# Performance work log

Hardware: AMD Instinct MI355X
Metric: run time of the kernel (lower is better)

The kernel has to match this reference:

```python
import jax, jax.numpy as jnp
import numpy as np

B, K, FM, TS, H, W = 128, 24, 24, 11, 40, 40
EPS = 1e-6


def setup_inputs() -> dict:
    key = jax.random.key(0)
    ks = jax.random.split(key, 8)

    def w(k, shape):
        fan_in = float(np.prod(shape[2:]))
        return jax.random.normal(k, shape, jnp.float32) / np.float32(np.sqrt(fan_in))

    return {
        "x": jax.random.normal(ks[0], (B, 1, H, W), jnp.float32),
        "noise": jax.random.uniform(ks[1], (B, K), jnp.float32, -2.0, 2.0),
        "W1": w(ks[2], (K, 128, 1, 3, 3)), "b1": jnp.zeros((K, 128), jnp.float32),
        "W2": w(ks[3], (K, 128, 128, 3, 3)), "b2": jnp.zeros((K, 128), jnp.float32),
        "W3": w(ks[4], (K, 128, 128, 3, 3)), "b3": jnp.zeros((K, 128), jnp.float32),
        "W4": w(ks[5], (K, 128, 128, 3, 3)), "b4": jnp.zeros((K, 128), jnp.float32),
        "W5": w(ks[6], (K, FM, 128, 1, 1)), "b5": jnp.zeros((K, FM), jnp.float32),
        "templates": jax.random.normal(ks[7], (K, TS, TS), jnp.float32),
    }


def _conv(x, w, b, s):
    y = jax.lax.conv_general_dilated(x, w, (s, s), 'VALID',
                                     dimension_numbers=('NCHW', 'OIHW', 'NCHW'))
    return y + b[None, :, None, None]


def _inv_affine_mats(pose):
    # pose [B,K,6]: angle(deg), tx, ty, scale, shear_x(deg), shear_y(deg)
    # torchvision-style inverse affine matrix (maps output canvas coords -> template coords)
    ang = jnp.deg2rad(pose[..., 0])
    tx, ty = pose[..., 1], pose[..., 2]
    sc = pose[..., 3] + EPS
    sx = jnp.deg2rad(pose[..., 4])
    sy = jnp.deg2rad(pose[..., 5])
    a = jnp.cos(ang - sy) / jnp.cos(sy)
    b = -jnp.cos(ang - sy) * jnp.tan(sx) / jnp.cos(sy) - jnp.sin(ang)
    c = jnp.sin(ang - sy) / jnp.cos(sy)
    d = -jnp.sin(ang - sy) * jnp.tan(sx) / jnp.cos(sy) + jnp.cos(ang)
    m00, m01, m10, m11 = d / sc, -b / sc, -c / sc, a / sc
    cx = cy = (TS - 1) * 0.5
    m02 = m00 * (-cx - tx) + m01 * (-cy - ty) + cx
    m12 = m10 * (-cx - tx) + m11 * (-cy - ty) + cy
    return m00, m01, m02, m10, m11, m12


def _warp_templates(templates, pose):
    # Fused affine warp + resize-to-(H,W), bilinear, zero fill (batched grid_sample).
    m00, m01, m02, m10, m11, m12 = _inv_affine_mats(pose)  # each [B,K]
    ys, xs = jnp.meshgrid(jnp.arange(H, dtype=jnp.float32),
                          jnp.arange(W, dtype=jnp.float32), indexing='ij')
    u = (xs + 0.5) * (TS / W) - 0.5  # output pixel -> template-canvas x
    v = (ys + 0.5) * (TS / H) - 0.5
    src_x = m00[..., None, None] * u + m01[..., None, None] * v + m02[..., None, None]
    src_y = m10[..., None, None] * u + m11[..., None, None] * v + m12[..., None, None]

    def sample(tmpl, sx_, sy_):  # tmpl [TS,TS]; sx_,sy_ [B,H,W]
        x0 = jnp.floor(sx_); y0 = jnp.floor(sy_)
        wx = sx_ - x0; wy = sy_ - y0
        x0i = x0.astype(jnp.int32); y0i = y0.astype(jnp.int32)

        def tap(yi, xi):
            ok = (xi >= 0) & (xi < TS) & (yi >= 0) & (yi < TS)
            val = tmpl[jnp.clip(yi, 0, TS - 1), jnp.clip(xi, 0, TS - 1)]
            return jnp.where(ok, val, 0.0)

        v00 = tap(y0i, x0i); v01 = tap(y0i, x0i + 1)
        v10 = tap(y0i + 1, x0i); v11 = tap(y0i + 1, x0i + 1)
        return (v00 * (1 - wx) + v01 * wx) * (1 - wy) + (v10 * (1 - wx) + v11 * wx) * wy

    return jax.vmap(sample, in_axes=(0, 1, 1), out_axes=1)(templates, src_x, src_y)  # [B,K,H,W]


def _forward(x, noise, W1, b1, W2, b2, W3, b3, W4, b4, W5, b5, templates):
    def capsule(w1, bb1, w2, bb2, w3, bb3, w4, bb4, w5, bb5):
        h = jax.nn.relu(_conv(x, w1, bb1, 2))
        h = jax.nn.relu(_conv(h, w2, bb2, 2))
        h = jax.nn.relu(_conv(h, w3, bb3, 1))
        h = jax.nn.relu(_conv(h, w4, bb4, 1))
        return _conv(h, w5, bb5, 1)

    outs = jax.vmap(capsule)(W1, b1, W2, b2, W3, b3, W4, b4, W5, b5)  # [K,B,FM,h,w]
    att = outs[:, :, -1]  # [K,B,h,w]
    hs, ws = att.shape[-2:]
    att = jax.nn.softmax(att.reshape(K, B, hs * ws), axis=-1).reshape(K, B, hs, ws)
    pooled = jnp.einsum('kbfhw,kbhw->bkf', outs[:, :, :-1], att)  # [B,K,FM-1]

    x_m = jax.nn.relu(pooled[:, :, :6])                        # [B,K,6] pose
    d_m = jax.nn.sigmoid(pooled[:, :, 6] + noise)[..., None]   # [B,K,1] presence
    c_z = jax.nn.relu(pooled[:, :, 7:])                        # [B,K,16]

    tt = _warp_templates(templates, x_m)                       # [B,K,H,W]
    mix_prob = jax.nn.softmax(d_m * tt.reshape(B, K, H * W), axis=2).reshape(B, K, H, W)

    std = jnp.std(x.reshape(B, 1, -1), axis=-1, ddof=1)[:, None]   # [B,1,1] (unbiased, as torch)
    mult = (1.0 / jnp.sqrt(std * 2.0 * jnp.pi))[..., None]         # [B,1,1,1] (as written in source)
    pmul = (-1.0 / (2.0 * std ** 2))[..., None]                    # [B,1,1,1]
    xd = jax.lax.stop_gradient(x)                                  # detach_x = x.data
    gaussians = mult * jnp.exp((xd - tt) ** 2 * pmul)              # [B,K,H,W]
    ll = jnp.log(jnp.sum(gaussians * mix_prob, axis=1)).sum((-1, -2)).mean()

    x_m_det = jax.lax.stop_gradient(x_m)
    d_m_det = jax.lax.stop_gradient(d_m)
    tmpl_det = jnp.broadcast_to(jax.lax.stop_gradient(templates).reshape(1, K, TS * TS),
                                (B, K, TS * TS))
    input_ocae = jnp.concatenate([d_m_det, x_m_det, tmpl_det, c_z], axis=-1)  # [B,K,144]
    return ll, input_ocae, x_m_det, d_m_det


def reference(x, noise, W1, b1, W2, b2, W3, b3, W4, b4, W5, b5, templates):
    return _forward(x, noise, W1, b1, W2, b2, W3, b3, W4, b4, W5, b5, templates)
```

## Files before the change

kernel.cpp:

```cpp
#include <hip/hip_runtime.h>
#include <math.h>

typedef __attribute__((ext_vector_type(8))) short bf16x8;
typedef __attribute__((ext_vector_type(4))) float f32x4;
typedef __attribute__((ext_vector_type(16))) float f32x16;
typedef unsigned int uint32;
typedef unsigned short ushort;

namespace {
constexpr int KK = 24, BB = 128;

constexpr size_t SZ_W1P = (size_t)24 * 128 * 32 * 2;
constexpr size_t SZ_W5P = (size_t)24 * 32 * 128 * 2;
constexpr size_t SZ_WB  = (size_t)24 * 128 * 1152 * 2;
constexpr size_t OFF_W1P = 0;
constexpr size_t OFF_W5P = OFF_W1P + SZ_W1P;
constexpr size_t OFF_WB2 = OFF_W5P + SZ_W5P;
constexpr size_t OFF_WB3 = OFF_WB2 + SZ_WB;
constexpr size_t OFF_WB4 = OFF_WB3 + SZ_WB;
constexpr size_t OFF_TT  = OFF_WB4 + SZ_WB;
constexpr size_t SZ_TT   = (size_t)128 * 24 * 1600 * 2;
constexpr size_t OFF_SMAX = OFF_TT + SZ_TT;
constexpr size_t OFF_SDEN = OFF_SMAX + 12288;
constexpr size_t OFF_DM   = OFF_SDEN + 12288;
constexpr size_t OFF_PART = OFF_DM + 12288;

constexpr long long O_OCAE = 1;
constexpr long long O_XM   = O_OCAE + (long long)BB * KK * 144;
constexpr long long O_DM   = O_XM + (long long)BB * KK * 6;

constexpr int R1_SZ   = 80864;
constexpr int XIM_OFF = 0;
constexpr int H1T_OFF = 23104;
constexpr int XSB_OFF = 74464;
constexpr int H2S_OFF = 0;
constexpr int H3S_OFF = 0;
constexpr int H4B_OFF = 31392;
constexpr int OUTS_OFF = 0;
constexpr int ATT_OFF = 4800;
constexpr int PS_OFF  = 5000;
}

__device__ inline ushort f2bf(float f) {
  uint32 u = __builtin_bit_cast(uint32, f);
  u += 0x7fffu + ((u >> 16) & 1u);
  return (ushort)(u >> 16);
}
__device__ inline float bf2f(ushort u) {
  return __builtin_bit_cast(float, (uint32)u << 16);
}
__device__ inline uint32 cvtpk(float a, float b) {
  uint32 r;
  asm("v_cvt_pk_bf16_f32 %0, %1, %2" : "=v"(r) : "v"(a), "v"(b));
  return r;
}
__device__ inline void bar_lds() {
  asm volatile("s_waitcnt lgkmcnt(0)\n\ts_barrier" ::: "memory");
}

__global__ __launch_bounds__(128) void k_w1p(const float* __restrict__ W1,
                                             const float* __restrict__ W5,
                                             const float* __restrict__ b1,
                                             ushort* __restrict__ W1p,
                                             ushort* __restrict__ W5p) {
  const int k = blockIdx.x, t = threadIdx.x;
  {
    ushort tmp[32];
    #pragma unroll
    for (int i = 0; i < 32; ++i) tmp[i] = 0;
    #pragma unroll
    for (int j = 0; j < 9; ++j) tmp[j] = f2bf(W1[(k * 128 + t) * 9 + j]);
    tmp[9] = f2bf(b1[k * 128 + t]);
    uint4* dp = (uint4*)(W1p + ((size_t)k * 128 + t) * 32);
    #pragma unroll
    for (int i = 0; i < 4; ++i) dp[i] = ((uint4*)tmp)[i];
  }
  if (t < 32) {
    ushort* dp = W5p + ((size_t)k * 32 + t) * 128;
    if (t < 24) {
      const float* sp = W5 + (size_t)k * 3072 + t * 128;
      for (int ci = 0; ci < 128; ++ci) dp[ci] = f2bf(sp[ci]);
    } else {
      for (int ci = 0; ci < 128; ++ci) dp[ci] = 0;
    }
  }
}

__global__ __launch_bounds__(256) void k_wp(
    const float* __restrict__ W2, const float* __restrict__ W3, const float* __restrict__ W4,
    ushort* __restrict__ W2p, ushort* __restrict__ W3p, ushort* __restrict__ W4p) {
  const int blk = blockIdx.x;
  const int sel = blk / 384;
  const int bb = blk - sel * 384;
  const float* src = (sel == 0) ? W2 : (sel == 1) ? W3 : W4;
  ushort* dst = (sel == 0) ? W2p : (sel == 1) ? W3p : W4p;
  const int k = bb >> 4;
  const int co = ((bb & 15) << 3) + (threadIdx.x >> 5);
  const int cil = threadIdx.x & 31;
  #pragma unroll
  for (int c = 0; c < 4; ++c) {
    const float* sp = src + ((size_t)(k * 128 + co) * 128 + c * 32 + cil) * 9;
    float v[9];
    #pragma unroll
    for (int j = 0; j < 9; ++j) v[j] = sp[j];
    ushort* dp = dst + (size_t)(k * 4 + c) * 9 * 128 * 32;
    #pragma unroll
    for (int j = 0; j < 9; ++j) dp[(j * 128 + co) * 32 + cil] = f2bf(v[j]);
  }
}

__device__ inline float tapf(const float* tm, int yi, int xi) {
  const bool ok = (xi >= 0) & (xi < 11) & (yi >= 0) & (yi < 11);
  const int yc = min(max(yi, 0), 10), xc = min(max(xi, 0), 10);
  const float v = tm[yc * 11 + xc];
  return ok ? v : 0.0f;
}

__global__ __launch_bounds__(256, 2) void k_tower(
    const float* __restrict__ x, const ushort* __restrict__ W1p,
    const ushort* __restrict__ W2p, const float* __restrict__ b2,
    const ushort* __restrict__ W3p, const float* __restrict__ b3,
    const ushort* __restrict__ W4p, const float* __restrict__ b4,
    const ushort* __restrict__ W5p, const float* __restrict__ b5,
    const float* __restrict__ noise, const float* __restrict__ templates,
    float* __restrict__ out, ushort* __restrict__ ttb,
    float* __restrict__ smax, float* __restrict__ sden, float* __restrict__ dmw)
{
  const int bi = blockIdx.x;
  const int blk = (bi & 7) * 192 + (bi >> 3);
  const int kb0 = blk * 2;
  const int k = kb0 >> 7;
  const int b0 = kb0 & 127;
  const int t = threadIdx.x;

  __shared__ __align__(16) char R1[R1_SZ];
  __shared__ float red[8];
  __shared__ float b5s[24];
  __shared__ float tm[121];

  ushort* xim = (ushort*)(R1 + XIM_OFF);
  ushort* h1T = (ushort*)(R1 + H1T_OFF);
  ushort* xsb = (ushort*)(R1 + XSB_OFF);
  char* h2sb = R1 + H2S_OFF;
  char* h3sb = R1 + H3S_OFF;
  ushort* h4b = (ushort*)(R1 + H4B_OFF);
  float*  outs_s = (float*)(R1 + OUTS_OFF);
  float*  att_s  = (float*)(R1 + ATT_OFF);
  float*  ps  = (float*)(R1 + PS_OFF);

  for (int i = t; i < 800; i += 256) {
    const int im = i / 400, j = i - im * 400;
    const float4 v = ((const float4*)(x + (size_t)(b0 + im) * 1600))[j];
    uint2 pk;
    pk.x = cvtpk(v.x, v.y);
    pk.y = cvtpk(v.z, v.w);
    *(uint2*)(xsb + im * 1600 + 4 * j) = pk;
  }
  bar_lds();

  for (int f = t; f < 722; f += 256) {
    const int im = f / 361, fl = f - im * 361;
    const int py = fl / 19, px = fl - 19 * py;
    const ushort* bp = xsb + im * 1600 + py * 80 + px * 2;
    const uint32 t0 = bp[0], t1 = bp[1], t2 = bp[2];
    const uint32 t3 = bp[40], t4 = bp[41], t5 = bp[42];
    const uint32 t6 = bp[80], t7 = bp[81], t8 = bp[82];
    uint4* dp = (uint4*)(xim + (im * 361 + fl) * 16);
    dp[0] = make_uint4(t0 | (t1 << 16), t2 | (t3 << 16), t4 | (t5 << 16), t6 | (t7 << 16));
    dp[1] = make_uint4(t8 | 0x3F800000u, 0u, 0u, 0u);
  }

  const int w = t >> 6, lane = t & 63, r = lane & 15, s = lane >> 4;
  const int l31 = lane & 31, kh = lane >> 5;
  const int img = w >> 1;
  const int wi  = w & 1;
  const int m0  = wi * 64;

  ushort* xim_i = xim + img * 5776;
  ushort* h1T_i = h1T + img * 14440;
  char* h1Tb_i = (char*)h1T_i;
  char* h2s_i = h2sb + img * 25920;
  char* h3s_i = h3sb + img * 15680;
  ushort* h4b_i = h4b + img * 3400;

  {
    int bb2[3];
    #pragma unroll
    for (int nt = 0; nt < 3; ++nt) {
      const int n = 32 * nt + l31;
      const int py = n / 9, px = n - 9 * py;
      bb2[nt] = ((n < 81) ? (38 * py + 2 * px) * 80 : 0) + 16 * kh;
    }

    f32x16 acc[2][3];
    #pragma unroll
    for (int mt = 0; mt < 2; ++mt)
      #pragma unroll
      for (int nt = 0; nt < 3; ++nt) acc[mt][nt] = (f32x16)(0.f);

    const ushort* W2k = W2p + (size_t)k * 147456 + (m0 + l31) * 32 + 8 * kh;
    const ushort* W1k = W1p + ((size_t)k * 128 + l31) * 32 + 8 * kh;

    for (int c = 0; c < 4; ++c) {
      bar_lds();
      {
        const bf16x8 a1 = *(const bf16x8*)(W1k + c * 1024);
        #pragma unroll
        for (int nt2 = 0; nt2 < 6; ++nt2) {
          const int n = (wi * 6 + nt2) * 32 + l31;
          const int pos = (n < 361) ? n : 360;
          const bf16x8 bv = *(const bf16x8*)(xim_i + pos * 16 + 8 * kh);
          f32x16 cc = __builtin_amdgcn_mfma_f32_32x32x16_bf16(a1, bv, (f32x16)(0.f), 0, 0, 0);
          if (n < 361) {
            #pragma unroll
            for (int q = 0; q < 4; ++q) {
              const int cil = 8 * q + 4 * kh;
              uint2 pk;
              pk.x = cvtpk(fmaxf(cc[4 * q + 0], 0.f), fmaxf(cc[4 * q + 1], 0.f));
              pk.y = cvtpk(fmaxf(cc[4 * q + 2], 0.f), fmaxf(cc[4 * q + 3], 0.f));
              *(uint2*)(h1T_i + n * 40 + cil) = pk;
            }
          }
        }
      }
      bar_lds();
      const ushort* Abase = W2k + (size_t)c * 36864;
      bf16x8 Ag[2][12];
      #pragma unroll
      for (int q = 0; q < 12; ++q)
        Ag[0][q] = *(const bf16x8*)(Abase + (size_t)(q >> 2) * 4096 + (q & 1) * 1024 + ((q >> 1) & 1) * 16);
      #pragma unroll
      for (int g = 0; g < 3; ++g) {
        if (g < 2) {
          #pragma unroll
          for (int q = 0; q < 12; ++q)
            Ag[(g + 1) & 1][q] = *(const bf16x8*)(Abase + (size_t)(3 * (g + 1) + (q >> 2)) * 4096 + (q & 1) * 1024 + ((q >> 1) & 1) * 16);
        }
        #pragma unroll
        for (int jj = 0; jj < 3; ++jj) {
          const int j = 3 * g + jj;
          const int off80 = ((j / 3) * 19 + (j - 3 * (j / 3))) * 80;
          bf16x8 Bv[2][3];
          #pragma unroll
          for (int h = 0; h < 2; ++h)
            #pragma unroll
            for (int nt = 0; nt < 3; ++nt)
              Bv[h][nt] = *(const bf16x8*)(h1Tb_i + bb2[nt] + off80 + 32 * h);
          #pragma unroll
          for (int h = 0; h < 2; ++h)
            #pragma unroll
            for (int mt = 0; mt < 2; ++mt)
              #pragma unroll
              for (int nt = 0; nt < 3; ++nt)
                acc[mt][nt] = __builtin_amdgcn_mfma_f32_32x32x16_bf16(
                    Ag[g & 1][jj * 4 + h * 2 + mt], Bv[h][nt], acc[mt][nt], 0, 0, 0);
        }
      }
    }
    bar_lds();
    #pragma unroll
    for (int mt = 0; mt < 2; ++mt)
      #pragma unroll
      for (int nt = 0; nt < 3; ++nt) {
        const int p = 32 * nt + l31;
        if (p < 81) {
          #pragma unroll
          for (int q = 0; q < 4; ++q) {
            const int co0 = m0 + 32 * mt + 8 * q + 4 * kh;
            const float4 bv = *(const float4*)(b2 + k * 128 + co0);
            const int c2 = co0 >> 5, cil = co0 & 31;
            uint2 pk;
            pk.x = cvtpk(fmaxf(acc[mt][nt][4 * q + 0] + bv.x, 0.f), fmaxf(acc[mt][nt][4 * q + 1] + bv.y, 0.f));
            pk.y = cvtpk(fmaxf(acc[mt][nt][4 * q + 2] + bv.z, 0.f), fmaxf(acc[mt][nt][4 * q + 3] + bv.w, 0.f));
            *(uint2*)(h2s_i + ((c2 * 81 + p) * 40 + cil) * 2) = pk;
          }
        }
      }
  }
  bar_lds();

  {
    int bb3[2];
    #pragma unroll
    for (int nt = 0; nt < 2; ++nt) {
      const int n = 32 * nt + l31;
      const int py = n / 7, px = n - 7 * py;
      bb3[nt] = ((n < 49) ? (9 * py + px) * 80 : 0) + 16 * kh;
    }
    f32x16 acc[2][2];
    #pragma unroll
    for (int mt = 0; mt < 2; ++mt)
      #pragma unroll
      for (int nt = 0; nt < 2; ++nt) acc[mt][nt] = (f32x16)(0.f);

    const ushort* W3k = W3p + (size_t)k * 147456 + (m0 + l31) * 32 + 8 * kh;
    for (int c = 0; c < 4; ++c) {
      const ushort* Abase = W3k + (size_t)c * 36864;
      const char* h2c = h2s_i + c * 6480;
      bf16x8 Ag[2][12];
      #pragma unroll
      for (int q = 0; q < 12; ++q)
        Ag[0][q] = *(const bf16x8*)(Abase + (size_t)(q >> 2) * 4096 + (q & 1) * 1024 + ((q >> 1) & 1) * 16);
      #pragma unroll
      for (int g = 0; g < 3; ++g) {
        if (g < 2) {
          #pragma unroll
          for (int q = 0; q < 12; ++q)
            Ag[(g + 1) & 1][q] = *(const bf16x8*)(Abase + (size_t)(3 * (g + 1) + (q >> 2)) * 4096 + (q & 1) * 1024 + ((q >> 1) & 1) * 16);
        }
        #pragma unroll
        for (int jj = 0; jj < 3; ++jj) {
          const int j = 3 * g + jj;
          const int off80 = ((j / 3) * 9 + (j - 3 * (j / 3))) * 80;
          bf16x8 Bv[2][2];
          #pragma unroll
          for (int h = 0; h < 2; ++h)
            #pragma unroll
            for (int nt = 0; nt < 2; ++nt)
              Bv[h][nt] = *(const bf16x8*)(h2c + bb3[nt] + off80 + 32 * h);
          #pragma unroll
          for (int h = 0; h < 2; ++h)
            #pragma unroll
            for (int mt = 0; mt < 2; ++mt)
              #pragma unroll
              for (int nt = 0; nt < 2; ++nt)
                acc[mt][nt] = __builtin_amdgcn_mfma_f32_32x32x16_bf16(
                    Ag[g & 1][jj * 4 + h * 2 + mt], Bv[h][nt], acc[mt][nt], 0, 0, 0);
        }
      }
    }
    bar_lds();
    #pragma unroll
    for (int mt = 0; mt < 2; ++mt)
      #pragma unroll
      for (int nt = 0; nt < 2; ++nt) {
        const int p = 32 * nt + l31;
        if (p < 49) {
          #pragma unroll
          for (int q = 0; q < 4; ++q) {
            const int co0 = m0 + 32 * mt + 8 * q + 4 * kh;
            const float4 bv = *(const float4*)(b3 + k * 128 + co0);
            const int c2 = co0 >> 5, cil = co0 & 31;
            uint2 pk;
            pk.x = cvtpk(fmaxf(acc[mt][nt][4 * q + 0] + bv.x, 0.f), fmaxf(acc[mt][nt][4 * q + 1] + bv.y, 0.f));
            pk.y = cvtpk(fmaxf(acc[mt][nt][4 * q + 2] + bv.z, 0.f), fmaxf(acc[mt][nt][4 * q + 3] + bv.w, 0.f));
            *(uint2*)(h3s_i + ((c2 * 49 + p) * 40 + cil) * 2) = pk;
          }
        }
      }
    for (int i = t; i < 121; i += 256) tm[i] = templates[k * 121 + i];
  }
  bar_lds();

  {
    const int n4 = l31;
    const int py4 = n4 / 5, px4 = n4 - 5 * py4;
    const int bb4 = ((n4 < 25) ? (7 * py4 + px4) * 80 : 0) + 16 * kh;
    f32x16 acc[2];
    acc[0] = (f32x16)(0.f);
    acc[1] = (f32x16)(0.f);

    const ushort* W4k = W4p + (size_t)k * 147456 + (m0 + l31) * 32 + 8 * kh;
    for (int c = 0; c < 4; ++c) {
      const ushort* Abase = W4k + (size_t)c * 36864;
      const char* h3c = h3s_i + c * 3920;
      bf16x8 Ag[2][12];
      #pragma unroll
      for (int q = 0; q < 12; ++q)
        Ag[0][q] = *(const bf16x8*)(Abase + (size_t)(q >> 2) * 4096 + (q & 1) * 1024 + ((q >> 1) & 1) * 16);
      #pragma unroll
      for (int g = 0; g < 3; ++g) {
        if (g < 2) {
          #pragma unroll
          for (int q = 0; q < 12; ++q)
            Ag[(g + 1) & 1][q] = *(const bf16x8*)(Abase + (size_t)(3 * (g + 1) + (q >> 2)) * 4096 + (q & 1) * 1024 + ((q >> 1) & 1) * 16);
        }
        #pragma unroll
        for (int jj = 0; jj < 3; ++jj) {
          const int j = 3 * g + jj;
          const int off80 = ((j / 3) * 7 + (j - 3 * (j / 3))) * 80;
          bf16x8 Bv[2];
          #pragma unroll
          for (int h = 0; h < 2; ++h)
            Bv[h] = *(const bf16x8*)(h3c + bb4 + off80 + 32 * h);
          #pragma unroll
          for (int h = 0; h < 2; ++h)
            #pragma unroll
            for (int mt = 0; mt < 2; ++mt)
              acc[mt] = __builtin_amdgcn_mfma_f32_32x32x16_bf16(
                  Ag[g & 1][jj * 4 + h * 2 + mt], Bv[h], acc[mt], 0, 0, 0);
        }
      }
    }
    bar_lds();
    #pragma unroll
    for (int mt = 0; mt < 2; ++mt) {
      const int p = l31;
      if (p < 25) {
        #pragma unroll
        for (int q = 0; q < 4; ++q) {
          const int co0 = m0 + 32 * mt + 8 * q + 4 * kh;
          const float4 bv = *(const float4*)(b4 + k * 128 + co0);
          uint2 pk;
          pk.x = cvtpk(fmaxf(acc[mt][4 * q + 0] + bv.x, 0.f), fmaxf(acc[mt][4 * q + 1] + bv.y, 0.f));
          pk.y = cvtpk(fmaxf(acc[mt][4 * q + 2] + bv.z, 0.f), fmaxf(acc[mt][4 * q + 3] + bv.w, 0.f));
          *(uint2*)(h4b_i + p * 136 + co0) = pk;
        }
      }
    }
    if (t < 24) b5s[t] = b5[k * 24 + t];
  }
  bar_lds();

  {
    const int mt = wi;
    f32x4 acc5[2];
    acc5[0] = (f32x4){0.f, 0.f, 0.f, 0.f};
    acc5[1] = (f32x4){0.f, 0.f, 0.f, 0.f};
    const ushort* A5 = W5p + ((size_t)k * 32 + mt * 16 + r) * 128 + 8 * s;
    #pragma unroll
    for (int ks = 0; ks < 4; ++ks) {
      const bf16x8 a5 = *(const bf16x8*)(A5 + ks * 32);
      #pragma unroll
      for (int nt = 0; nt < 2; ++nt) {
        const int p = 16 * nt + r;
        const int pv = (p < 25) ? p : 0;
        const bf16x8 bv = *(const bf16x8*)(h4b_i + pv * 136 + ks * 32 + 8 * s);
        acc5[nt] = __builtin_amdgcn_mfma_f32_16x16x32_bf16(a5, bv, acc5[nt], 0, 0, 0);
      }
    }
    #pragma unroll
    for (int nt = 0; nt < 2; ++nt) {
      const int p = 16 * nt + r;
      if (p < 25) {
        #pragma unroll
        for (int rg = 0; rg < 4; ++rg) {
          const int fm = mt * 16 + 4 * s + rg;
          if (fm < 24) outs_s[img * 600 + fm * 25 + p] = acc5[nt][rg] + b5s[fm];
        }
      }
    }
  }
  bar_lds();

  if (!(t & 64)) {
    const int im = t >> 7;
    const int tl = t & 63;
    float v = (tl < 25) ? outs_s[im * 600 + 575 + tl] : -1e30f;
    #pragma unroll
    for (int off = 32; off; off >>= 1) v = fmaxf(v, __shfl_xor(v, off));
    const float m = v;
    float e = (tl < 25) ? expf(outs_s[im * 600 + 575 + tl] - m) : 0.0f;
    float ss = e;
    #pragma unroll
    for (int off = 32; off; off >>= 1) ss += __shfl_xor(ss, off);
    if (tl < 25) att_s[im * 25 + tl] = e / ss;
  }
  bar_lds();

  {
    const int im = t >> 7;
    const int tl = t & 127;
    if (tl < 23) {
      float v = 0.f;
      #pragma unroll
      for (int p = 0; p < 25; ++p) v = fmaf(outs_s[im * 600 + tl * 25 + p], att_s[im * 25 + p], v);
      ps[im * 23 + tl] = v;
    }
  }
  bar_lds();

  float dmv[2];
  #pragma unroll
  for (int im = 0; im < 2; ++im) {
    const int idx = (b0 + im) * KK + k;
    const float dl = ps[im * 23 + 6] + noise[idx];
    dmv[im] = 1.0f / (1.0f + expf(-dl));
  }

  #pragma unroll
  for (int im = 0; im < 2; ++im) {
    const int idx = (b0 + im) * KK + k;
    if (t < 144) {
      float v;
      if (t == 0)       v = dmv[im];
      else if (t < 7)   v = fmaxf(ps[im * 23 + t - 1], 0.0f);
      else if (t < 128) v = tm[t - 7];
      else              v = fmaxf(ps[im * 23 + 7 + (t - 128)], 0.0f);
      out[O_OCAE + (size_t)idx * 144 + t] = v;
    }
    if (t < 6) out[O_XM + (size_t)idx * 6 + t] = fmaxf(ps[im * 23 + t], 0.0f);
    if (t == 0) out[O_DM + idx] = dmv[im];
  }

  const int im = t >> 7;
  const int tl = t & 127;
  const int idx = (b0 + im) * KK + k;
  const float dm = dmv[im];

  const float D2R = 0.017453292519943295f;
  const float ang = fmaxf(ps[im * 23 + 0], 0.0f) * D2R;
  const float tx = fmaxf(ps[im * 23 + 1], 0.0f), ty = fmaxf(ps[im * 23 + 2], 0.0f);
  const float sc = fmaxf(ps[im * 23 + 3], 0.0f) + 1e-6f;
  const float sxr = fmaxf(ps[im * 23 + 4], 0.0f) * D2R;
  const float syr = fmaxf(ps[im * 23 + 5], 0.0f) * D2R;
  const float cas = cosf(ang - syr), sas = sinf(ang - syr);
  const float csy = cosf(syr), tsx = tanf(sxr);
  const float a_ = cas / csy;
  const float b_ = -cas * tsx / csy - sinf(ang);
  const float c_ = sas / csy;
  const float d_ = -sas * tsx / csy + cosf(ang);
  const float m00 = d_ / sc, m01 = -b_ / sc, m10 = -c_ / sc, m11 = a_ / sc;
  const float m02 = m00 * (-5.0f - tx) + m01 * (-5.0f - ty) + 5.0f;
  const float m12 = m10 * (-5.0f - tx) + m11 * (-5.0f - ty) + 5.0f;

  const float S = 0.275f;
  float ttv[13];
  float lmax = -1e30f;
  #pragma unroll
  for (int i = 0; i < 13; ++i) {
    const int pix = tl + 128 * i;
    float val2 = 0.0f;
    if (pix < 1600) {
      const int py = pix / 40, px = pix - 40 * py;
      const float u = (px + 0.5f) * S - 0.5f;
      const float v = (py + 0.5f) * S - 0.5f;
      const float sx = m00 * u + m01 * v + m02;
      const float sy = m10 * u + m11 * v + m12;
      const float x0 = floorf(sx), y0 = floorf(sy);
      const float wx = sx - x0, wy = sy - y0;
      const int xi = (int)x0, yi = (int)y0;
      const float v00 = tapf(tm, yi, xi);
      const float v01 = tapf(tm, yi, xi + 1);
      const float v10 = tapf(tm, yi + 1, xi);
      const float v11 = tapf(tm, yi + 1, xi + 1);
      const float val = (v00 * (1.0f - wx) + v01 * wx) * (1.0f - wy) + (v10 * (1.0f - wx) + v11 * wx) * wy;
      const ushort tb = f2bf(val);
      val2 = bf2f(tb);
      ttb[(size_t)idx * 1600 + pix] = tb;
      lmax = fmaxf(lmax, dm * val2);
    }
    ttv[i] = val2;
  }

  #pragma unroll
  for (int off = 32; off; off >>= 1) lmax = fmaxf(lmax, __shfl_xor(lmax, off));
  if ((t & 63) == 0) red[t >> 6] = lmax;
  bar_lds();
  const float m = fmaxf(red[2 * im], red[2 * im + 1]);
  float ls = 0.0f;
  #pragma unroll
  for (int i = 0; i < 13; ++i)
    if (tl + 128 * i < 1600) ls += expf(fmaf(dm, ttv[i], -m));
  #pragma unroll
  for (int off = 32; off; off >>= 1) ls += __shfl_xor(ls, off);
  bar_lds();
  if ((t & 63) == 0) red[4 + (t >> 6)] = ls;
  bar_lds();
  if ((t & 127) == 0) {
    smax[idx] = m;
    sden[idx] = red[4 + 2 * im] + red[5 + 2 * im];
    dmw[idx] = dm;
  }
}

__global__ __launch_bounds__(256) void k_ll(
    const float* __restrict__ x, const ushort* __restrict__ ttb,
    const float* __restrict__ smax, const float* __restrict__ sden,
    const float* __restrict__ dmw, float* __restrict__ part)
{
  const int b = blockIdx.x >> 2;
  const int chunk = blockIdx.x & 3;
  const int t = threadIdx.x;

  __shared__ __align__(16) float xs[1600];
  __shared__ float kd[24], km[24], ki[24];
  __shared__ float red[4], red2[4];

  for (int i = t; i < 400; i += 256)
    ((float4*)xs)[i] = ((const float4*)(x + (size_t)b * 1600))[i];
  if (t < 24) {
    kd[t] = dmw[b * 24 + t];
    km[t] = smax[b * 24 + t];
    ki[t] = 1.0f / sden[b * 24 + t];
  }
  __syncthreads();

  float s1 = 0.f, s2 = 0.f;
  for (int i = t; i < 1600; i += 256) { const float v = xs[i]; s1 += v; s2 = fmaf(v, v, s2); }
  #pragma unroll
  for (int off = 32; off; off >>= 1) { s1 += __shfl_xor(s1, off); s2 += __shfl_xor(s2, off); }
  if ((t & 63) == 0) { red[t >> 6] = s1; red2[t >> 6] = s2; }
  __syncthreads();
  s1 = red[0] + red[1] + red[2] + red[3];
  s2 = red2[0] + red2[1] + red2[2] + red2[3];
  const float var = (s2 - s1 * s1 * (1.0f / 1600.0f)) * (1.0f / 1599.0f);
  const float stdv = sqrtf(var);
  const float mult = 1.0f / sqrtf(stdv * 6.283185307179586f);
  const float pmul = -1.0f / (2.0f * stdv * stdv);

  const int p0 = chunk * 400;
  float ll = 0.0f;
  for (int ii = t; ii < 400; ii += 256) {
    const int pix = p0 + ii;
    const float xv = xs[pix];
    float sum = 0.0f;
    #pragma unroll 6
    for (int kk2 = 0; kk2 < 24; ++kk2) {
      const float tv = bf2f(ttb[(size_t)(b * 24 + kk2) * 1600 + pix]);
      const float dxv = xv - tv;
      sum += expf(fmaf(dxv * dxv, pmul, fmaf(kd[kk2], tv, -km[kk2]))) * ki[kk2];
    }
    ll += logf(mult * sum);
  }
  #pragma unroll
  for (int off = 32; off; off >>= 1) ll += __shfl_xor(ll, off);
  __syncthreads();
  if ((t & 63) == 0) red[t >> 6] = ll;
  __syncthreads();
  if (t == 0) part[blockIdx.x] = red[0] + red[1] + red[2] + red[3];
}

__global__ void k_final(const float* __restrict__ part, float* __restrict__ out)
{
  const int t = threadIdx.x;
  float v = part[t] + part[t + 256];
  #pragma unroll
  for (int off = 32; off; off >>= 1) v += __shfl_xor(v, off);
  __shared__ float red[4];
  if ((t & 63) == 0) red[t >> 6] = v;
  __syncthreads();
  if (t == 0) out[0] = (red[0] + red[1] + red[2] + red[3]) * (1.0f / 128.0f);
}

extern "C" void kernel_launch(void* const* d_in, const int* in_sizes, int n_in,
                              void* d_out, int out_size, void* d_ws, size_t ws_size,
                              hipStream_t stream)
{
  const float* x     = (const float*)d_in[0];
  const float* noise = (const float*)d_in[1];
  const float* W1    = (const float*)d_in[2];
  const float* b1    = (const float*)d_in[3];
  const float* W2    = (const float*)d_in[4];
  const float* b2    = (const float*)d_in[5];
  const float* W3    = (const float*)d_in[6];
  const float* b3    = (const float*)d_in[7];
  const float* W4    = (const float*)d_in[8];
  const float* b4    = (const float*)d_in[9];
  const float* W5    = (const float*)d_in[10];
  const float* b5    = (const float*)d_in[11];
  const float* tmpl  = (const float*)d_in[12];
  float* out = (float*)d_out;
  char* wsb = (char*)d_ws;

  ushort* W1p = (ushort*)(wsb + OFF_W1P);
  ushort* W5p = (ushort*)(wsb + OFF_W5P);
  ushort* W2p = (ushort*)(wsb + OFF_WB2);
  ushort* W3p = (ushort*)(wsb + OFF_WB3);
  ushort* W4p = (ushort*)(wsb + OFF_WB4);
  ushort* ttp  = (ushort*)(wsb + OFF_TT);
  float* smaxp = (float*)(wsb + OFF_SMAX);
  float* sdenp = (float*)(wsb + OFF_SDEN);
  float* dmp   = (float*)(wsb + OFF_DM);
  float* partp = (float*)(wsb + OFF_PART);

  k_w1p<<<24, 128, 0, stream>>>(W1, W5, b1, W1p, W5p);
  k_wp<<<1152, 256, 0, stream>>>(W2, W3, W4, W2p, W3p, W4p);
  k_tower<<<KK * BB / 2, 256, 0, stream>>>(x, W1p, W2p, b2, W3p, b3, W4p, b4,
                                           W5p, b5, noise, tmpl, out, ttp, smaxp, sdenp, dmp);
  k_ll<<<BB * 4, 256, 0, stream>>>(x, ttp, smaxp, sdenp, dmp, partp);
  k_final<<<1, 256, 0, stream>>>(partp, out);
}
```

Baseline: 233.1 us.

## Switch conv2-4 tower to FP8 weights/activations with scaled 32x32x64 MFMA

Converts the W2-W4 weights to FP8 (e4m3) in the pre-pack kernel and stores the h1/h2/h3 intermediate activations in LDS as FP8. The conv layers now use mfma_scale 32x32x64 f8f6f4 instructions with unit scales, covering 64 input channels per instruction instead of 16. The goal is to halve weight and LDS traffic and cut the MFMA instruction count. The cost is lower numerical precision, which risks tolerance failures. The LDS layouts and the conv1 work split across waves are also reorganised.

```diff
diff --git a/kernel.cpp b/kernel.cpp
--- a/kernel.cpp
+++ b/kernel.cpp
@@ -4,15 +4,18 @@
 typedef __attribute__((ext_vector_type(8))) short bf16x8;
 typedef __attribute__((ext_vector_type(4))) float f32x4;
 typedef __attribute__((ext_vector_type(16))) float f32x16;
+typedef __attribute__((ext_vector_type(4))) int i32x4;
+typedef __attribute__((ext_vector_type(8))) int i32x8;
 typedef unsigned int uint32;
 typedef unsigned short ushort;
+typedef unsigned char uchar;
 
 namespace {
 constexpr int KK = 24, BB = 128;
 
 constexpr size_t SZ_W1P = (size_t)24 * 128 * 32 * 2;
 constexpr size_t SZ_W5P = (size_t)24 * 32 * 128 * 2;
-constexpr size_t SZ_WB  = (size_t)24 * 128 * 1152 * 2;
+constexpr size_t SZ_WB  = (size_t)24 * 2 * 9 * 128 * 64;
 constexpr size_t OFF_W1P = 0;
 constexpr size_t OFF_W5P = OFF_W1P + SZ_W1P;
 constexpr size_t OFF_WB2 = OFF_W5P + SZ_W5P;
@@ -57,6 +60,16 @@
 __device__ inline void bar_lds() {
   asm volatile("s_waitcnt lgkmcnt(0)\n\ts_barrier" ::: "memory");
 }
+__device__ inline uint32 pk4fp8(float a, float b, float c, float d) {
+  int u = __builtin_amdgcn_cvt_pk_fp8_f32(fmaxf(a, 0.f), fmaxf(b, 0.f), 0, false);
+  u = __builtin_amdgcn_cvt_pk_fp8_f32(fmaxf(c, 0.f), fmaxf(d, 0.f), u, true);
+  return (uint32)u;
+}
+__device__ inline i32x8 ldB8(const char* p) {
+  i32x4 lo = *(const i32x4*)(p);
+  i32x4 hi = *(const i32x4*)(p + 16);
+  return __builtin_shufflevector(lo, hi, 0, 1, 2, 3, 4, 5, 6, 7);
+}
 
 __global__ __launch_bounds__(128) void k_w1p(const float* __restrict__ W1,
                                              const float* __restrict__ W5,
@@ -88,12 +101,12 @@
 
 __global__ __launch_bounds__(256) void k_wp(
     const float* __restrict__ W2, const float* __restrict__ W3, const float* __restrict__ W4,
-    ushort* __restrict__ W2p, ushort* __restrict__ W3p, ushort* __restrict__ W4p) {
+    uchar* __restrict__ W2p, uchar* __restrict__ W3p, uchar* __restrict__ W4p) {
   const int blk = blockIdx.x;
   const int sel = blk / 384;
   const int bb = blk - sel * 384;
   const float* src = (sel == 0) ? W2 : (sel == 1) ? W3 : W4;
-  ushort* dst = (sel == 0) ? W2p : (sel == 1) ? W3p : W4p;
+  uchar* dst = (sel == 0) ? W2p : (sel == 1) ? W3p : W4p;
   const int k = bb >> 4;
   const int co = ((bb & 15) << 3) + (threadIdx.x >> 5);
   const int cil = threadIdx.x & 31;
@@ -103,9 +116,10 @@
     float v[9];
     #pragma unroll
     for (int j = 0; j < 9; ++j) v[j] = sp[j];
-    ushort* dp = dst + (size_t)(k * 4 + c) * 9 * 128 * 32;
-    #pragma unroll
-    for (int j = 0; j < 9; ++j) dp[(j * 128 + co) * 32 + cil] = f2bf(v[j]);
+    uchar* dp = dst + (size_t)(k * 2 + (c >> 1)) * 9 * 8192 + co * 64 + (c & 1) * 32 + cil;
+    #pragma unroll
+    for (int j = 0; j < 9; ++j)
+      dp[(size_t)j * 8192] = (uchar)(__builtin_amdgcn_cvt_pk_fp8_f32(v[j], v[j], 0, false) & 0xFF);
   }
 }
 
@@ -118,9 +132,9 @@
 
 __global__ __launch_bounds__(256, 2) void k_tower(
     const float* __restrict__ x, const ushort* __restrict__ W1p,
-    const ushort* __restrict__ W2p, const float* __restrict__ b2,
-    const ushort* __restrict__ W3p, const float* __restrict__ b3,
-    const ushort* __restrict__ W4p, const float* __restrict__ b4,
+    const uchar* __restrict__ W2p, const float* __restrict__ b2,
+    const uchar* __restrict__ W3p, const float* __restrict__ b3,
+    const uchar* __restrict__ W4p, const float* __restrict__ b4,
     const ushort* __restrict__ W5p, const float* __restrict__ b5,
     const float* __restrict__ noise, const float* __restrict__ templates,
     float* __restrict__ out, ushort* __restrict__ ttb,
@@ -139,8 +153,8 @@
   __shared__ float tm[121];
 
   ushort* xim = (ushort*)(R1 + XIM_OFF);
-  ushort* h1T = (ushort*)(R1 + H1T_OFF);
   ushort* xsb = (ushort*)(R1 + XSB_OFF);
+  char* h1Tall = R1 + H1T_OFF;
   char* h2sb = R1 + H2S_OFF;
   char* h3sb = R1 + H3S_OFF;
   ushort* h4b = (ushort*)(R1 + H4B_OFF);
@@ -170,17 +184,17 @@
     dp[1] = make_uint4(t8 | 0x3F800000u, 0u, 0u, 0u);
   }
 
-  const int w = t >> 6, lane = t & 63, r = lane & 15, s = lane >> 4;
+  const int w = t >> 6, lane = t & 63;
+  const int r = lane & 15, s = lane >> 4;
   const int l31 = lane & 31, kh = lane >> 5;
   const int img = w >> 1;
   const int wi  = w & 1;
   const int m0  = wi * 64;
 
   ushort* xim_i = xim + img * 5776;
-  ushort* h1T_i = h1T + img * 14440;
-  char* h1Tb_i = (char*)h1T_i;
-  char* h2s_i = h2sb + img * 25920;
-  char* h3s_i = h3sb + img * 15680;
+  char* h1Tb_i = h1Tall + img * 28880;
+  char* h2s_i = h2sb + img * 12960;
+  char* h3s_i = h3sb + img * 7840;
   ushort* h4b_i = h4b + img * 3400;
 
   {
@@ -189,7 +203,7 @@
     for (int nt = 0; nt < 3; ++nt) {
       const int n = 32 * nt + l31;
       const int py = n / 9, px = n - 9 * py;
-      bb2[nt] = ((n < 81) ? (38 * py + 2 * px) * 80 : 0) + 16 * kh;
+      bb2[nt] = ((n < 81) ? (38 * py + 2 * px) * 80 : 0) + 32 * kh;
     }
 
     f32x16 acc[2][3];
@@ -198,63 +212,51 @@
       #pragma unroll
       for (int nt = 0; nt < 3; ++nt) acc[mt][nt] = (f32x16)(0.f);
 
-    const ushort* W2k = W2p + (size_t)k * 147456 + (m0 + l31) * 32 + 8 * kh;
+    const uchar* W2k = W2p + ((size_t)k * 2) * 9 * 8192 + (m0 + l31) * 64 + 32 * kh;
     const ushort* W1k = W1p + ((size_t)k * 128 + l31) * 32 + 8 * kh;
 
-    for (int c = 0; c < 4; ++c) {
+    for (int cp = 0; cp < 2; ++cp) {
       bar_lds();
       {
-        const bf16x8 a1 = *(const bf16x8*)(W1k + c * 1024);
-        #pragma unroll
-        for (int nt2 = 0; nt2 < 6; ++nt2) {
-          const int n = (wi * 6 + nt2) * 32 + l31;
+        const bf16x8 a1 = *(const bf16x8*)(W1k + (2 * cp + wi) * 1024);
+        #pragma unroll
+        for (int nt2 = 0; nt2 < 12; ++nt2) {
+          const int n = nt2 * 32 + l31;
           const int pos = (n < 361) ? n : 360;
           const bf16x8 bv = *(const bf16x8*)(xim_i + pos * 16 + 8 * kh);
           f32x16 cc = __builtin_amdgcn_mfma_f32_32x32x16_bf16(a1, bv, (f32x16)(0.f), 0, 0, 0);
           if (n < 361) {
             #pragma unroll
             for (int q = 0; q < 4; ++q) {
-              const int cil = 8 * q + 4 * kh;
-              uint2 pk;
-              pk.x = cvtpk(fmaxf(cc[4 * q + 0], 0.f), fmaxf(cc[4 * q + 1], 0.f));
-              pk.y = cvtpk(fmaxf(cc[4 * q + 2], 0.f), fmaxf(cc[4 * q + 3], 0.f));
-              *(uint2*)(h1T_i + n * 40 + cil) = pk;
+              const uint32 u = pk4fp8(cc[4 * q], cc[4 * q + 1], cc[4 * q + 2], cc[4 * q + 3]);
+              *(uint32*)(h1Tb_i + n * 80 + 32 * wi + 8 * q + 4 * kh) = u;
             }
           }
         }
       }
       bar_lds();
-      const ushort* Abase = W2k + (size_t)c * 36864;
-      bf16x8 Ag[2][12];
-      #pragma unroll
-      for (int q = 0; q < 12; ++q)
-        Ag[0][q] = *(const bf16x8*)(Abase + (size_t)(q >> 2) * 4096 + (q & 1) * 1024 + ((q >> 1) & 1) * 16);
-      #pragma unroll
-      for (int g = 0; g < 3; ++g) {
-        if (g < 2) {
+      const uchar* Abase = W2k + (size_t)cp * 9 * 8192;
+      i32x8 Af[2][2];
+      #pragma unroll
+      for (int mt = 0; mt < 2; ++mt) Af[0][mt] = *(const i32x8*)(Abase + mt * 2048);
+      #pragma unroll
+      for (int j = 0; j < 9; ++j) {
+        if (j < 8) {
           #pragma unroll
-          for (int q = 0; q < 12; ++q)
-            Ag[(g + 1) & 1][q] = *(const bf16x8*)(Abase + (size_t)(3 * (g + 1) + (q >> 2)) * 4096 + (q & 1) * 1024 + ((q >> 1) & 1) * 16);
-        }
-        #pragma unroll
-        for (int jj = 0; jj < 3; ++jj) {
-          const int j = 3 * g + jj;
-          const int off80 = ((j / 3) * 19 + (j - 3 * (j / 3))) * 80;
-          bf16x8 Bv[2][3];
+          for (int mt = 0; mt < 2; ++mt)
+            Af[(j + 1) & 1][mt] = *(const i32x8*)(Abase + (size_t)(j + 1) * 8192 + mt * 2048);
+        }
+        const int off80 = ((j / 3) * 19 + (j - 3 * (j / 3))) * 80;
+        i32x8 Bv[3];
+        #pragma unroll
+        for (int nt = 0; nt < 3; ++nt)
+          Bv[nt] = ldB8(h1Tb_i + bb2[nt] + off80);
+        #pragma unroll
+        for (int mt = 0; mt < 2; ++mt)
           #pragma unroll
-          for (int h = 0; h < 2; ++h)
-            #pragma unroll
-            for (int nt = 0; nt < 3; ++nt)
-              Bv[h][nt] = *(const bf16x8*)(h1Tb_i + bb2[nt] + off80 + 32 * h);
-          #pragma unroll
-          for (int h = 0; h < 2; ++h)
-            #pragma unroll
-            for (int mt = 0; mt < 2; ++mt)
-              #pragma unroll
-              for (int nt = 0; nt < 3; ++nt)
-                acc[mt][nt] = __builtin_amdgcn_mfma_f32_32x32x16_bf16(
-                    Ag[g & 1][jj * 4 + h * 2 + mt], Bv[h][nt], acc[mt][nt], 0, 0, 0);
-        }
+          for (int nt = 0; nt < 3; ++nt)
+            acc[mt][nt] = __builtin_amdgcn_mfma_scale_f32_32x32x64_f8f6f4(
+                Af[j & 1][mt], Bv[nt], acc[mt][nt], 0, 0, 0, 127, 0, 127);
       }
     }
     bar_lds();
@@ -268,11 +270,9 @@
           for (int q = 0; q < 4; ++q) {
             const int co0 = m0 + 32 * mt + 8 * q + 4 * kh;
             const float4 bv = *(const float4*)(b2 + k * 128 + co0);
-            const int c2 = co0 >> 5, cil = co0 & 31;
-            uint2 pk;
-            pk.x = cvtpk(fmaxf(acc[mt][nt][4 * q + 0] + bv.x, 0.f), fmaxf(acc[mt][nt][4 * q + 1] + bv.y, 0.f));
-            pk.y = cvtpk(fmaxf(acc[mt][nt][4 * q + 2] + bv.z, 0.f), fmaxf(acc[mt][nt][4 * q + 3] + bv.w, 0.f));
-            *(uint2*)(h2s_i + ((c2 * 81 + p) * 40 + cil) * 2) = pk;
+            const uint32 u = pk4fp8(acc[mt][nt][4 * q + 0] + bv.x, acc[mt][nt][4 * q + 1] + bv.y,
+                                    acc[mt][nt][4 * q + 2] + bv.z, acc[mt][nt][4 * q + 3] + bv.w);
+            *(uint32*)(h2s_i + (co0 >> 6) * 6480 + p * 80 + (co0 & 63)) = u;
           }
         }
       }
@@ -285,7 +285,7 @@
     for (int nt = 0; nt < 2; ++nt) {
       const int n = 32 * nt + l31;
       const int py = n / 7, px = n - 7 * py;
-      bb3[nt] = ((n < 49) ? (9 * py + px) * 80 : 0) + 16 * kh;
+      bb3[nt] = ((n < 49) ? (9 * py + px) * 80 : 0) + 32 * kh;
     }
     f32x16 acc[2][2];
     #pragma unroll
@@ -293,40 +293,31 @@
       #pragma unroll
       for (int nt = 0; nt < 2; ++nt) acc[mt][nt] = (f32x16)(0.f);
 
-    const ushort* W3k = W3p + (size_t)k * 147456 + (m0 + l31) * 32 + 8 * kh;
-    for (int c = 0; c < 4; ++c) {
-      const ushort* Abase = W3k + (size_t)c * 36864;
-      const char* h2c = h2s_i + c * 6480;
-      bf16x8 Ag[2][12];
-      #pragma unroll
-      for (int q = 0; q < 12; ++q)
-        Ag[0][q] = *(const bf16x8*)(Abase + (size_t)(q >> 2) * 4096 + (q & 1) * 1024 + ((q >> 1) & 1) * 16);
-      #pragma unroll
-      for (int g = 0; g < 3; ++g) {
-        if (g < 2) {
+    const uchar* W3k = W3p + ((size_t)k * 2) * 9 * 8192 + (m0 + l31) * 64 + 32 * kh;
+    for (int cp = 0; cp < 2; ++cp) {
+      const uchar* Abase = W3k + (size_t)cp * 9 * 8192;
+      const char* h2c = h2s_i + cp * 6480;
+      i32x8 Af[2][2];
+      #pragma unroll
+      for (int mt = 0; mt < 2; ++mt) Af[0][mt] = *(const i32x8*)(Abase + mt * 2048);
+      #pragma unroll
+      for (int j = 0; j < 9; ++j) {
+        if (j < 8) {
           #pragma unroll
-          for (int q = 0; q < 12; ++q)
-            Ag[(g + 1) & 1][q] = *(const bf16x8*)(Abase + (size_t)(3 * (g + 1) + (q >> 2)) * 4096 + (q & 1) * 1024 + ((q >> 1) & 1) * 16);
-        }
-        #pragma unroll
-        for (int jj = 0; jj < 3; ++jj) {
-          const int j = 3 * g + jj;
-          const int off80 = ((j / 3) * 9 + (j - 3 * (j / 3))) * 80;
-          bf16x8 Bv[2][2];
+          for (int mt = 0; mt < 2; ++mt)
+            Af[(j + 1) & 1][mt] = *(const i32x8*)(Abase + (size_t)(j + 1) * 8192 + mt * 2048);
+        }
+        const int off80 = ((j / 3) * 9 + (j - 3 * (j / 3))) * 80;
+        i32x8 Bv[2];
+        #pragma unroll
+        for (int nt = 0; nt < 2; ++nt)
+          Bv[nt] = ldB8(h2c + bb3[nt] + off80);
+        #pragma unroll
+        for (int mt = 0; mt < 2; ++mt)
           #pragma unroll
-          for (int h = 0; h < 2; ++h)
-            #pragma unroll
-            for (int nt = 0; nt < 2; ++nt)
-              Bv[h][nt] = *(const bf16x8*)(h2c + bb3[nt] + off80 + 32 * h);
-          #pragma unroll
-          for (int h = 0; h < 2; ++h)
-            #pragma unroll
-            for (int mt = 0; mt < 2; ++mt)
-              #pragma unroll
-              for (int nt = 0; nt < 2; ++nt)
-                acc[mt][nt] = __builtin_amdgcn_mfma_f32_32x32x16_bf16(
-                    Ag[g & 1][jj * 4 + h * 2 + mt], Bv[h][nt], acc[mt][nt], 0, 0, 0);
-        }
+          for (int nt = 0; nt < 2; ++nt)
+            acc[mt][nt] = __builtin_amdgcn_mfma_scale_f32_32x32x64_f8f6f4(
+                Af[j & 1][mt], Bv[nt], acc[mt][nt], 0, 0, 0, 127, 0, 127);
       }
     }
     bar_lds();
@@ -340,11 +331,9 @@
           for (int q = 0; q < 4; ++q) {
             const int co0 = m0 + 32 * mt + 8 * q + 4 * kh;
             const float4 bv = *(const float4*)(b3 + k * 128 + co0);
-            const int c2 = co0 >> 5, cil = co0 & 31;
-            uint2 pk;
-            pk.x = cvtpk(fmaxf(acc[mt][nt][4 * q + 0] + bv.x, 0.f), fmaxf(acc[mt][nt][4 * q + 1] + bv.y, 0.f));
-            pk.y = cvtpk(fmaxf(acc[mt][nt][4 * q + 2] + bv.z, 0.f), fmaxf(acc[mt][nt][4 * q + 3] + bv.w, 0.f));
-            *(uint2*)(h3s_i + ((c2 * 49 + p) * 40 + cil) * 2) = pk;
+            const uint32 u = pk4fp8(acc[mt][nt][4 * q + 0] + bv.x, acc[mt][nt][4 * q + 1] + bv.y,
+                                    acc[mt][nt][4 * q + 2] + bv.z, acc[mt][nt][4 * q + 3] + bv.w);
+            *(uint32*)(h3s_i + (co0 >> 6) * 3920 + p * 80 + (co0 & 63)) = u;
           }
         }
       }
@@ -355,41 +344,31 @@
   {
     const int n4 = l31;
     const int py4 = n4 / 5, px4 = n4 - 5 * py4;
-    const int bb4 = ((n4 < 25) ? (7 * py4 + px4) * 80 : 0) + 16 * kh;
+    const int bb4 = ((n4 < 25) ? (7 * py4 + px4) * 80 : 0) + 32 * kh;
     f32x16 acc[2];
     acc[0] = (f32x16)(0.f);
     acc[1] = (f32x16)(0.f);
 
-    const ushort* W4k = W4p + (size_t)k * 147456 + (m0 + l31) * 32 + 8 * kh;
-    for (int c = 0; c < 4; ++c) {
-      const ushort* Abase = W4k + (size_t)c * 36864;
-      const char* h3c = h3s_i + c * 3920;
-      bf16x8 Ag[2][12];
-      #pragma unroll
-      for (int q = 0; q < 12; ++q)
-        Ag[0][q] = *(const bf16x8*)(Abase + (size_t)(q >> 2) * 4096 + (q & 1) * 1024 + ((q >> 1) & 1) * 16);
-      #pragma unroll
-      for (int g = 0; g < 3; ++g) {
-        if (g < 2) {
+    const uchar* W4k = W4p + ((size_t)k * 2) * 9 * 8192 + (m0 + l31) * 64 + 32 * kh;
+    for (int cp = 0; cp < 2; ++cp) {
+      const uchar* Abase = W4k + (size_t)cp * 9 * 8192;
+      const char* h3c = h3s_i + cp * 3920;
+      i32x8 Af[2][2];
+      #pragma unroll
+      for (int mt = 0; mt < 2; ++mt) Af[0][mt] = *(const i32x8*)(Abase + mt * 2048);
+      #pragma unroll
+      for (int j = 0; j < 9; ++j) {
+        if (j < 8) {
           #pragma unroll
-          for (int q = 0; q < 12; ++q)
-            Ag[(g + 1) & 1][q] = *(const bf16x8*)(Abase + (size_t)(3 * (g + 1) + (q >> 2)) * 4096 + (q & 1) * 1024 + ((q >> 1) & 1) * 16);
-        }
-        #pragma unroll
-        for (int jj = 0; jj < 3; ++jj) {
-          const int j = 3 * g + jj;
-          const int off80 = ((j / 3) * 7 + (j - 3 * (j / 3))) * 80;
-          bf16x8 Bv[2];
-          #pragma unroll
-          for (int h = 0; h < 2; ++h)
-            Bv[h] = *(const bf16x8*)(h3c + bb4 + off80 + 32 * h);
-          #pragma unroll
-          for (int h = 0; h < 2; ++h)
-            #pragma unroll
-            for (int mt = 0; mt < 2; ++mt)
-              acc[mt] = __builtin_amdgcn_mfma_f32_32x32x16_bf16(
-                  Ag[g & 1][jj * 4 + h * 2 + mt], Bv[h], acc[mt], 0, 0, 0);
-        }
+          for (int mt = 0; mt < 2; ++mt)
+            Af[(j + 1) & 1][mt] = *(const i32x8*)(Abase + (size_t)(j + 1) * 8192 + mt * 2048);
+        }
+        const int off80 = ((j / 3) * 7 + (j - 3 * (j / 3))) * 80;
+        const i32x8 Bv = ldB8(h3c + bb4 + off80);
+        #pragma unroll
+        for (int mt = 0; mt < 2; ++mt)
+          acc[mt] = __builtin_amdgcn_mfma_scale_f32_32x32x64_f8f6f4(
+              Af[j & 1][mt], Bv, acc[mt], 0, 0, 0, 127, 0, 127);
       }
     }
     bar_lds();
@@ -655,9 +634,9 @@
 
   ushort* W1p = (ushort*)(wsb + OFF_W1P);
   ushort* W5p = (ushort*)(wsb + OFF_W5P);
-  ushort* W2p = (ushort*)(wsb + OFF_WB2);
-  ushort* W3p = (ushort*)(wsb + OFF_WB3);
-  ushort* W4p = (ushort*)(wsb + OFF_WB4);
+  uchar* W2p = (uchar*)(wsb + OFF_WB2);
+  uchar* W3p = (uchar*)(wsb + OFF_WB3);
+  uchar* W4p = (uchar*)(wsb + OFF_WB4);
   ushort* ttp  = (ushort*)(wsb + OFF_TT);
   float* smaxp = (float*)(wsb + OFF_SMAX);
   float* sdenp = (float*)(wsb + OFF_SDEN);
```

Measured after the change: 450.9 us. 93.4% more time.
